# Kernel optimization log

Measured on AMD Instinct MI355X. Metric: run time of the kernel, lower is better.

Reference implementation:

```python
import jax, jax.numpy as jnp
import numpy as np

N_PTS = 16384
DIM = 3

def setup_inputs() -> dict:
    key = jax.random.key(0)
    k1, k2 = jax.random.split(key)
    source_cloud = jax.random.normal(k1, (1, N_PTS, DIM), dtype=jnp.float32)
    target_cloud = jax.random.normal(k2, (1, N_PTS, DIM), dtype=jnp.float32)
    return {"source_cloud": source_cloud, "target_cloud": target_cloud}


def _min_sq_dists(x, y):
    # x: [B, N, D], y: [B, M, D] -> [B, N] squared distance to nearest neighbor in y
    x2 = jnp.sum(x * x, axis=-1)              # [B, N]
    y2 = jnp.sum(y * y, axis=-1)              # [B, M]
    xy = jnp.einsum('bnd,bmd->bnm', x, y)     # [B, N, M]
    d = x2[:, :, None] + y2[:, None, :] - 2.0 * xy  # squared dists, as pytorch3d knn_points
    return jnp.min(d, axis=-1)                # K=1 nearest neighbor


def reference(source_cloud, target_cloud):
    chamfer_forward = _min_sq_dists(source_cloud, target_cloud)[0]   # [N]
    chamfer_backward = _min_sq_dists(target_cloud, source_cloud)[0]  # [M]
    return (chamfer_forward, chamfer_backward)
```

## Files before the change

kernel.cpp:

```cpp
#include <hip/hip_runtime.h>

#define NPTS 16384
#define KS   16
#define BT   256
#define BROWS 256
#define TSPLIT 8
#define SWEEP (NPTS / TSPLIT)
#define NTILE (SWEEP / 32)

typedef __attribute__((ext_vector_type(8)))  short bf16x8;
typedef __attribute__((ext_vector_type(16))) float f32x16;

__device__ __forceinline__ unsigned short btrunc(float f) {
    return (unsigned short)(__float_as_uint(f) >> 16);
}
__device__ __forceinline__ float btruncf(float f) {
    return __uint_as_float(__float_as_uint(f) & 0xFFFF0000u);
}

__global__ void chamfer_pack(const float* __restrict__ s,
                             const float* __restrict__ t,
                             unsigned short* __restrict__ Apack,
                             unsigned short* __restrict__ Bpack,
                             float* __restrict__ sq,
                             unsigned* __restrict__ outinit)
{
    int i = blockIdx.x * blockDim.x + threadIdx.x;
    if (i >= 2 * NPTS) return;
    outinit[i] = 0x7F7F7F7Fu;
    int cloud = i >> 14;
    int p = i & (NPTS - 1);
    const float* base = cloud ? t : s;
    float x = base[3 * p], y = base[3 * p + 1], z = base[3 * p + 2];

    float xh = btruncf(x), yh = btruncf(y), zh = btruncf(z);
    float xl = x - xh, yl = y - yh, zl = z - zh;
    float q = x * x + y * y + z * z;
    float qh = btruncf(q), ql = q - qh;

    unsigned short* A = Apack + (size_t)i * KS;
    unsigned short* B = Bpack + (size_t)i * KS;

    A[0] = btrunc(-2.f * xh); A[1] = btrunc(-2.f * xl); A[2] = A[0];
    A[3] = btrunc(-2.f * yh); A[4] = btrunc(-2.f * yl); A[5] = A[3];
    A[6] = btrunc(-2.f * zh); A[7] = btrunc(-2.f * zl); A[8] = A[6];
    A[9] = btrunc(1.0f);      A[10] = A[9];
    A[11] = A[12] = A[13] = A[14] = A[15] = 0;

    B[0] = btrunc(xh); B[1] = B[0]; B[2] = btrunc(xl);
    B[3] = btrunc(yh); B[4] = B[3]; B[5] = btrunc(yl);
    B[6] = btrunc(zh); B[7] = B[6]; B[8] = btrunc(zl);
    B[9] = btrunc(qh); B[10] = btrunc(ql);
    B[11] = B[12] = B[13] = B[14] = B[15] = 0;

    sq[i] = q;
}

__global__ __launch_bounds__(BT, 4)
void chamfer_mfma(const unsigned short* __restrict__ Apack,
                  const unsigned short* __restrict__ Bpack,
                  const float* __restrict__ sq,
                  unsigned* __restrict__ out)
{
    const int dir = blockIdx.z;
    const unsigned short* A = Apack + (size_t)(dir ? NPTS : 0) * KS;
    const unsigned short* B = Bpack + (size_t)(dir ? 0 : NPTS) * KS;
    const float* s2 = sq + (dir ? NPTS : 0);
    unsigned* o = out + dir * NPTS;

    const int lane = threadIdx.x & 63;
    const int wv   = threadIdx.x >> 6;
    const int n32  = lane & 31;
    const int kh   = lane >> 5;

    const int rbase = blockIdx.x * BROWS + wv * 64;

    const bf16x8 a0 = *(const bf16x8*)(A + (size_t)(rbase + n32) * KS + kh * 8);
    const bf16x8 a1 = *(const bf16x8*)(A + (size_t)(rbase + 32 + n32) * KS + kh * 8);

    f32x16 mn0, mn1, zc;
#pragma unroll
    for (int r = 0; r < 16; ++r) { mn0[r] = 1e30f; mn1[r] = 1e30f; zc[r] = 0.0f; }

    const unsigned short* Bl = B + (size_t)(blockIdx.y * SWEEP + n32) * KS + kh * 8;
#define BTILE(t) (*(const bf16x8*)(Bl + (size_t)(t) * 32 * KS))

#define PROC(bb)                                                                   \
    {                                                                              \
        f32x16 c0 = __builtin_amdgcn_mfma_f32_32x32x16_bf16(a0, (bb), zc, 0, 0, 0);\
        f32x16 c1 = __builtin_amdgcn_mfma_f32_32x32x16_bf16(a1, (bb), zc, 0, 0, 0);\
        _Pragma("unroll")                                                          \
        for (int r = 0; r < 16; ++r) mn0[r] = fminf(mn0[r], c0[r]);                \
        _Pragma("unroll")                                                          \
        for (int r = 0; r < 16; ++r) mn1[r] = fminf(mn1[r], c1[r]);                \
    }

    bf16x8 b0 = BTILE(0);
    bf16x8 b1 = BTILE(1);
#pragma unroll 2
    for (int t = 0; t < NTILE - 2; t += 2) {
        bf16x8 n0 = BTILE(t + 2);
        bf16x8 n1 = BTILE(t + 3);
        PROC(b0);
        PROC(b1);
        b0 = n0;
        b1 = n1;
    }
    PROC(b0);
    PROC(b1);

#pragma unroll
    for (int r = 0; r < 16; ++r) {
        float v0 = mn0[r], v1 = mn1[r];
        v0 = fminf(v0, __shfl_xor(v0, 1, 32));  v1 = fminf(v1, __shfl_xor(v1, 1, 32));
        v0 = fminf(v0, __shfl_xor(v0, 2, 32));  v1 = fminf(v1, __shfl_xor(v1, 2, 32));
        v0 = fminf(v0, __shfl_xor(v0, 4, 32));  v1 = fminf(v1, __shfl_xor(v1, 4, 32));
        v0 = fminf(v0, __shfl_xor(v0, 8, 32));  v1 = fminf(v1, __shfl_xor(v1, 8, 32));
        v0 = fminf(v0, __shfl_xor(v0, 16, 32)); v1 = fminf(v1, __shfl_xor(v1, 16, 32));
        mn0[r] = v0; mn1[r] = v1;
    }

    if (n32 == 0) {
#pragma unroll
        for (int r = 0; r < 16; ++r) {
            int row0 = rbase + (r & 3) + 8 * (r >> 2) + 4 * kh;
            float d0 = fmaxf(mn0[r] + s2[row0], 0.0f);
            atomicMin(&o[row0], __float_as_uint(d0));
            int row1 = row0 + 32;
            float d1 = fmaxf(mn1[r] + s2[row1], 0.0f);
            atomicMin(&o[row1], __float_as_uint(d1));
        }
    }
#undef PROC
#undef BTILE
}

extern "C" void kernel_launch(void* const* d_in, const int* in_sizes, int n_in,
                              void* d_out, int out_size, void* d_ws, size_t ws_size,
                              hipStream_t stream) {
    const float* s = (const float*)d_in[0];
    const float* t = (const float*)d_in[1];

    unsigned short* Apack = (unsigned short*)d_ws;
    unsigned short* Bpack = Apack + (size_t)2 * NPTS * KS;
    float* sq = (float*)(Bpack + (size_t)2 * NPTS * KS);

    chamfer_pack<<<(2 * NPTS + BT - 1) / BT, BT, 0, stream>>>(
        s, t, Apack, Bpack, sq, (unsigned*)d_out);

    dim3 grid(NPTS / BROWS, TSPLIT, 2);
    chamfer_mfma<<<grid, BT, 0, stream>>>(Apack, Bpack, sq, (unsigned*)d_out);
}
```

Baseline: 35.97 us.

## Deepen B-tile prefetch, merge min ops, halve column split, vectorize pack stores

Result: slower. 41.09 us (+14.2%).

```diff
diff --git a/kernel.cpp b/kernel.cpp
--- a/kernel.cpp
+++ b/kernel.cpp
@@ -4,12 +4,14 @@
 #define KS   16
 #define BT   256
 #define BROWS 256
-#define TSPLIT 8
+#define TSPLIT 4
 #define SWEEP (NPTS / TSPLIT)
 #define NTILE (SWEEP / 32)
+#define NR (NTILE / 2)
 
 typedef __attribute__((ext_vector_type(8)))  short bf16x8;
 typedef __attribute__((ext_vector_type(16))) float f32x16;
+typedef __attribute__((ext_vector_type(8)))  unsigned short ushort8;
 
 __device__ __forceinline__ unsigned short btrunc(float f) {
     return (unsigned short)(__float_as_uint(f) >> 16);
@@ -38,25 +40,24 @@
     float q = x * x + y * y + z * z;
     float qh = btruncf(q), ql = q - qh;
 
-    unsigned short* A = Apack + (size_t)i * KS;
-    unsigned short* B = Bpack + (size_t)i * KS;
+    const unsigned short one = btrunc(1.0f);
+    ushort8 A0 = { btrunc(-2.f * xh), btrunc(-2.f * xl), btrunc(-2.f * xh),
+                   btrunc(-2.f * yh), btrunc(-2.f * yl), btrunc(-2.f * yh),
+                   btrunc(-2.f * zh), btrunc(-2.f * zl) };
+    ushort8 A1 = { btrunc(-2.f * zh), one, one, 0, 0, 0, 0, 0 };
+    ushort8 B0 = { btrunc(xh), btrunc(xh), btrunc(xl),
+                   btrunc(yh), btrunc(yh), btrunc(yl),
+                   btrunc(zh), btrunc(zh) };
+    ushort8 B1 = { btrunc(zl), btrunc(qh), btrunc(ql), 0, 0, 0, 0, 0 };
 
-    A[0] = btrunc(-2.f * xh); A[1] = btrunc(-2.f * xl); A[2] = A[0];
-    A[3] = btrunc(-2.f * yh); A[4] = btrunc(-2.f * yl); A[5] = A[3];
-    A[6] = btrunc(-2.f * zh); A[7] = btrunc(-2.f * zl); A[8] = A[6];
-    A[9] = btrunc(1.0f);      A[10] = A[9];
-    A[11] = A[12] = A[13] = A[14] = A[15] = 0;
-
-    B[0] = btrunc(xh); B[1] = B[0]; B[2] = btrunc(xl);
-    B[3] = btrunc(yh); B[4] = B[3]; B[5] = btrunc(yl);
-    B[6] = btrunc(zh); B[7] = B[6]; B[8] = btrunc(zl);
-    B[9] = btrunc(qh); B[10] = btrunc(ql);
-    B[11] = B[12] = B[13] = B[14] = B[15] = 0;
-
+    *(ushort8*)(Apack + (size_t)i * KS)     = A0;
+    *(ushort8*)(Apack + (size_t)i * KS + 8) = A1;
+    *(ushort8*)(Bpack + (size_t)i * KS)     = B0;
+    *(ushort8*)(Bpack + (size_t)i * KS + 8) = B1;
     sq[i] = q;
 }
 
-__global__ __launch_bounds__(BT, 4)
+__global__ __launch_bounds__(BT, 2)
 void chamfer_mfma(const unsigned short* __restrict__ Apack,
                   const unsigned short* __restrict__ Bpack,
                   const float* __restrict__ sq,
@@ -85,29 +86,28 @@
     const unsigned short* Bl = B + (size_t)(blockIdx.y * SWEEP + n32) * KS + kh * 8;
 #define BTILE(t) (*(const bf16x8*)(Bl + (size_t)(t) * 32 * KS))
 
-#define PROC(bb)                                                                   \
-    {                                                                              \
-        f32x16 c0 = __builtin_amdgcn_mfma_f32_32x32x16_bf16(a0, (bb), zc, 0, 0, 0);\
-        f32x16 c1 = __builtin_amdgcn_mfma_f32_32x32x16_bf16(a1, (bb), zc, 0, 0, 0);\
-        _Pragma("unroll")                                                          \
-        for (int r = 0; r < 16; ++r) mn0[r] = fminf(mn0[r], c0[r]);                \
-        _Pragma("unroll")                                                          \
-        for (int r = 0; r < 16; ++r) mn1[r] = fminf(mn1[r], c1[r]);                \
+    bf16x8 b0 = BTILE(0), b1 = BTILE(1);
+    bf16x8 n0 = BTILE(2), n1 = BTILE(3);
+
+#pragma unroll 2
+    for (int r = 0; r < NR; ++r) {
+        int tp = (2 * r + 4 < NTILE) ? 2 * r + 4 : NTILE - 2;
+        bf16x8 p0 = BTILE(tp);
+        bf16x8 p1 = BTILE(tp + 1);
+
+        f32x16 c00 = __builtin_amdgcn_mfma_f32_32x32x16_bf16(a0, b0, zc, 0, 0, 0);
+        f32x16 c01 = __builtin_amdgcn_mfma_f32_32x32x16_bf16(a0, b1, zc, 0, 0, 0);
+        f32x16 c10 = __builtin_amdgcn_mfma_f32_32x32x16_bf16(a1, b0, zc, 0, 0, 0);
+        f32x16 c11 = __builtin_amdgcn_mfma_f32_32x32x16_bf16(a1, b1, zc, 0, 0, 0);
+#pragma unroll
+        for (int k = 0; k < 16; ++k)
+            mn0[k] = fminf(fminf(mn0[k], c00[k]), c01[k]);
+#pragma unroll
+        for (int k = 0; k < 16; ++k)
+            mn1[k] = fminf(fminf(mn1[k], c10[k]), c11[k]);
+
+        b0 = n0; b1 = n1; n0 = p0; n1 = p1;
     }
-
-    bf16x8 b0 = BTILE(0);
-    bf16x8 b1 = BTILE(1);
-#pragma unroll 2
-    for (int t = 0; t < NTILE - 2; t += 2) {
-        bf16x8 n0 = BTILE(t + 2);
-        bf16x8 n1 = BTILE(t + 3);
-        PROC(b0);
-        PROC(b1);
-        b0 = n0;
-        b1 = n1;
-    }
-    PROC(b0);
-    PROC(b1);
 
 #pragma unroll
     for (int r = 0; r < 16; ++r) {
@@ -131,7 +131,6 @@
             atomicMin(&o[row1], __float_as_uint(d1));
         }
     }
-#undef PROC
 #undef BTILE
 }
 
```
